# Performance work log

Hardware: AMD Instinct MI355X
Metric: run time of the kernel (lower is better)

Reference implementation:

```python
import jax, jax.numpy as jnp
import numpy as np


def setup_inputs() -> dict:
    key = jax.random.key(0)
    ks = jax.random.split(key, 8)
    B, T, D, H = 4, 4096, 1024, 64
    scale = D ** -0.5
    return {
        "x": jax.random.normal(ks[0], (B, T, D), dtype=jnp.float32),
        "mask": jax.random.randint(ks[1], (B, T), 0, 2, dtype=jnp.int32),
        "wq": jax.random.normal(ks[2], (H, D), dtype=jnp.float32) * scale,
        "bq": jax.random.normal(ks[3], (H,), dtype=jnp.float32) * 0.02,
        "wk": jax.random.normal(ks[4], (H, D), dtype=jnp.float32) * scale,
        "bk": jax.random.normal(ks[5], (H,), dtype=jnp.float32) * 0.02,
        "wv": jax.random.normal(ks[6], (H, D), dtype=jnp.float32) * scale,
        "bv": jax.random.normal(ks[7], (H,), dtype=jnp.float32) * 0.02,
    }


def reference(x, mask, wq, bq, wk, bk, wv, bv):
    # x: [B,T,D]; wq/wk/wv: [H,D] (torch Linear convention), mask: [B,T] int
    head_size = wq.shape[0]
    q = jnp.einsum("btd,hd->bth", x, wq) + bq  # [B,T,H]
    k = jnp.einsum("btd,hd->bth", x, wk) + bk
    v = jnp.einsum("btd,hd->bth", x, wv) + bv
    attn = jnp.einsum("bth,bsh->bts", q, k) * (head_size ** -0.5)  # [B,T,T]
    pad_mask = mask.astype(bool)[:, None, :]  # [B,1,T], True = keep
    attn = jnp.where(pad_mask, attn, jnp.float32(-1e9))
    attn = jax.nn.softmax(attn, axis=-1)
    # dropout is identity in eval/deterministic mode
    return jnp.einsum("bts,bsh->bth", attn, v)  # [B,T,H]
```

## Files before the change

kernel.cpp:

```cpp
#include <hip/hip_runtime.h>
#include <math.h>

#define BATCH 4
#define SEQ   4096
#define DIM   1024
#define HEAD  64
#define MROWS (BATCH*SEQ)
#define NCOL  192
#define WST   1040
#define KT    64
#define QBLK  64
#define BK2   64
#define NIT2  (DIM / BK2)

typedef __attribute__((ext_vector_type(8))) short short8;
typedef __attribute__((ext_vector_type(4))) float f32x4;

static __device__ __forceinline__ unsigned short f2b(float f) {
    union { float f; unsigned u; } v; v.f = f;
    return (unsigned short)((v.u + 0x7FFFu + ((v.u >> 16) & 1u)) >> 16);
}
static __device__ __forceinline__ unsigned cvtpk(float a, float b) {
    unsigned r;
    asm("v_cvt_pk_bf16_f32 %0, %1, %2" : "=v"(r) : "v"(a), "v"(b));
    return r;
}

#define QSC (0.125f * 1.4426950408889634f)
__global__ __launch_bounds__(256) void wconv_kernel(
    const float* __restrict__ wq, const float* __restrict__ bq,
    const float* __restrict__ wk, const float* __restrict__ bk,
    const float* __restrict__ wv, const float* __restrict__ bv,
    unsigned short* __restrict__ Wb, float* __restrict__ biasAll)
{
    int idx = blockIdx.x * 256 + threadIdx.x;
    int e   = idx * 4;
    int row = e >> 10;
    int col = e & 1023;
    const float* src = (row < 64) ? wq : (row < 128) ? wk : wv;
    float s = (row < 64) ? QSC : 1.0f;
    float4 g = *(const float4*)&src[(size_t)(row & 63) * DIM + col];
    ushort4 o;
    o.x = f2b(g.x * s); o.y = f2b(g.y * s); o.z = f2b(g.z * s); o.w = f2b(g.w * s);
    *(ushort4*)&Wb[(size_t)row * WST + col] = o;
    if (idx < 192) {
        const float* bs = (idx < 64) ? bq : (idx < 128) ? bk : bv;
        biasAll[idx] = bs[idx & 63] * ((idx < 64) ? QSC : 1.0f);
    }
}

__global__ __launch_bounds__(256, 4) void qkvmm_kernel(
    const float* __restrict__ x, const unsigned short* __restrict__ Wb,
    const float* __restrict__ biasAll,
    unsigned short* __restrict__ qout, unsigned short* __restrict__ kout,
    unsigned short* __restrict__ vtout)
{
    __shared__ unsigned short xs[32 * BK2];
    __shared__ unsigned short ws[NCOL * BK2];

    const int tid  = threadIdx.x;
    const int m0   = blockIdx.x * 32;
    const int bb   = m0 >> 12;
    const int lane = tid & 63;
    const int w    = tid >> 6;
    const int lr   = lane & 15;
    const int lg   = lane >> 4;
    const int mrow  = (w >> 1) * 16;
    const int nbase = (w & 1) * 6;

    int wrow[6], wc[6];
    #pragma unroll
    for (int j = 0; j < 6; ++j) { int L = j * 256 + tid; wrow[j] = L >> 3; wc[j] = L & 7; }
    const int xr = tid >> 2, xq = tid & 3;

    f32x4 acc[6];
    #pragma unroll
    for (int nt = 0; nt < 6; ++nt) acc[nt] = (f32x4){0.f, 0.f, 0.f, 0.f};

    float4 xg[4];
    short8 wg[6];

    auto LOADR = [&](int ko) {
        if (tid < 128) {
            const float* xp = &x[(size_t)(m0 + xr) * DIM + ko + xq * 16];
            xg[0] = *(const float4*)xp;       xg[1] = *(const float4*)(xp + 4);
            xg[2] = *(const float4*)(xp + 8); xg[3] = *(const float4*)(xp + 12);
        }
        #pragma unroll
        for (int j = 0; j < 6; ++j)
            wg[j] = *(const short8*)&Wb[(size_t)wrow[j] * WST + ko + wc[j] * 8];
    };
    auto WRITE = [&]() {
        if (tid < 128) {
            uint4 c0, c1;
            c0.x = cvtpk(xg[0].x, xg[0].y); c0.y = cvtpk(xg[0].z, xg[0].w);
            c0.z = cvtpk(xg[1].x, xg[1].y); c0.w = cvtpk(xg[1].z, xg[1].w);
            c1.x = cvtpk(xg[2].x, xg[2].y); c1.y = cvtpk(xg[2].z, xg[2].w);
            c1.z = cvtpk(xg[3].x, xg[3].y); c1.w = cvtpk(xg[3].z, xg[3].w);
            *(uint4*)&xs[xr * BK2 + (((2 * xq)     ^ (xr & 7)) * 8)] = c0;
            *(uint4*)&xs[xr * BK2 + (((2 * xq + 1) ^ (xr & 7)) * 8)] = c1;
        }
        #pragma unroll
        for (int j = 0; j < 6; ++j)
            *(short8*)&ws[wrow[j] * BK2 + ((wc[j] ^ (wrow[j] & 7)) * 8)] = wg[j];
    };

    LOADR(0);
    for (int it = 0; it < NIT2; ++it) {
        __syncthreads();
        WRITE();
        __syncthreads();
        if (it + 1 < NIT2) LOADR((it + 1) * BK2);

        __builtin_amdgcn_s_setprio(1);
        #pragma unroll
        for (int h = 0; h < 2; ++h) {
            const int arow = mrow + lr;
            short8 af = *(const short8*)&xs[arow * BK2 + (((h * 4 + lg) ^ (arow & 7)) * 8)];
            #pragma unroll
            for (int nt = 0; nt < 6; ++nt) {
                int n = (nbase + nt) * 16 + lr;
                short8 bf = *(const short8*)&ws[n * BK2 + (((h * 4 + lg) ^ (n & 7)) * 8)];
                acc[nt] = __builtin_amdgcn_mfma_f32_16x16x32_bf16(af, bf, acc[nt], 0, 0, 0);
            }
        }
        __builtin_amdgcn_s_setprio(0);
    }

    #pragma unroll
    for (int nt = 0; nt < 6; ++nt) {
        int gn = (nbase + nt) * 16 + lr;
        float bv_ = biasAll[gn];
        #pragma unroll
        for (int r = 0; r < 4; ++r) {
            int grow = m0 + mrow + lg * 4 + r;
            unsigned short val = f2b(acc[nt][r] + bv_);
            if (gn < 64)       qout[(size_t)grow * HEAD + gn] = val;
            else if (gn < 128) kout[(size_t)grow * HEAD + gn - 64] = val;
            else {
                int t = (m0 & 4095) + mrow + lg * 4 + r;
                vtout[((size_t)bb * HEAD + gn - 128) * SEQ + t] = val;
            }
        }
    }
}

__global__ __launch_bounds__(256, 4) void flashmm_kernel(
    const unsigned short* __restrict__ qb, const unsigned short* __restrict__ kb,
    const unsigned short* __restrict__ vt, const int* __restrict__ mask,
    float* __restrict__ opart, float* __restrict__ mpart, float* __restrict__ lpart,
    int nsplit)
{
    const int b  = blockIdx.y;
    const int t0 = blockIdx.x * QBLK;
    const int z  = blockIdx.z;
    const int tid  = threadIdx.x;
    const int lane = tid & 63;
    const int w    = tid >> 6;
    const int lr = lane & 15;
    const int lg = lane >> 4;
    const int span = SEQ / nsplit;
    const int s_begin = z * span, s_end = s_begin + span;

    __shared__ unsigned short ks_l[KT * HEAD];
    __shared__ unsigned short vt_l[HEAD * KT];
    __shared__ unsigned short ps_l[4][16 * KT];
    __shared__ float mkf[KT];

    const unsigned short* qrow = qb + ((size_t)(b * SEQ + t0 + w * 16 + lr)) * HEAD;
    const short8 qf0 = *(const short8*)(qrow + lg * 8);
    const short8 qf1 = *(const short8*)(qrow + 32 + lg * 8);

    f32x4 acc_o[4];
    #pragma unroll
    for (int nt = 0; nt < 4; ++nt) acc_o[nt] = (f32x4){0.f, 0.f, 0.f, 0.f};
    float m_r = -INFINITY, l_r = 0.f;

    short8 kg[2], vg[2];
    float mgf = 0.f;

    auto LOADR = [&](int st) {
        #pragma unroll
        for (int i = 0; i < 2; ++i) {
            int c   = tid + i * 256;
            int row = c >> 3;
            int h0  = (c & 7) * 8;
            kg[i] = *(const short8*)(kb + ((size_t)(b * SEQ + st + row)) * HEAD + h0);
            vg[i] = *(const short8*)(vt + ((size_t)(b * HEAD + row)) * SEQ + st + h0);
        }
        if (tid < KT) mgf = (mask[(size_t)b * SEQ + st + tid] != 0) ? 0.f : -1e9f;
    };
    auto WRITE = [&]() {
        #pragma unroll
        for (int i = 0; i < 2; ++i) {
            int c   = tid + i * 256;
            int row = c >> 3;
            int h0  = (c & 7) * 8;
            *(short8*)&ks_l[row * HEAD + (h0 ^ ((row & 7) << 3))] = kg[i];
            *(short8*)&vt_l[row * KT + (h0 ^ ((row & 7) << 3))] = vg[i];
        }
        if (tid < KT) mkf[tid] = mgf;
    };

    LOADR(s_begin);
    for (int st = s_begin; st < s_end; st += KT) {
        __syncthreads();
        WRITE();
        __syncthreads();
        if (st + KT < s_end) LOADR(st + KT);

        f32x4 sT[4];
        __builtin_amdgcn_s_setprio(1);
        #pragma unroll
        for (int ct = 0; ct < 4; ++ct) {
            int krow = ct * 16 + lr;
            short8 kf0 = *(const short8*)&ks_l[krow * HEAD + ((lg * 8) ^ ((krow & 7) << 3))];
            short8 kf1 = *(const short8*)&ks_l[krow * HEAD + ((32 + lg * 8) ^ ((krow & 7) << 3))];
            f32x4 zz = (f32x4){0.f, 0.f, 0.f, 0.f};
            zz = __builtin_amdgcn_mfma_f32_16x16x32_bf16(kf0, qf0, zz, 0, 0, 0);
            zz = __builtin_amdgcn_mfma_f32_16x16x32_bf16(kf1, qf1, zz, 0, 0, 0);
            sT[ct] = zz;
        }
        __builtin_amdgcn_s_setprio(0);

        #pragma unroll
        for (int ct = 0; ct < 4; ++ct) {
            f32x4 mb = *(const f32x4*)&mkf[ct * 16 + lg * 4];
            sT[ct][0] += mb[0]; sT[ct][1] += mb[1];
            sT[ct][2] += mb[2]; sT[ct][3] += mb[3];
        }

        float mx = sT[0][0];
        #pragma unroll
        for (int ct = 0; ct < 4; ++ct)
            #pragma unroll
            for (int r = 0; r < 4; ++r) mx = fmaxf(mx, sT[ct][r]);
        mx = fmaxf(mx, __shfl_xor(mx, 16));
        mx = fmaxf(mx, __shfl_xor(mx, 32));

        bool defer = __all(mx <= m_r + 8.f);
        float base = defer ? m_r : fmaxf(m_r, mx);

        float rs = 0.f;
        #pragma unroll
        for (int ct = 0; ct < 4; ++ct)
            #pragma unroll
            for (int r = 0; r < 4; ++r) {
                float p = __builtin_amdgcn_exp2f(sT[ct][r] - base);
                sT[ct][r] = p;
                rs += p;
            }
        rs += __shfl_xor(rs, 16);
        rs += __shfl_xor(rs, 32);

        if (defer) {
            l_r += rs;
        } else {
            float sf = __builtin_amdgcn_exp2f(m_r - base);
            l_r = l_r * sf + rs;
            m_r = base;
            #pragma unroll
            for (int r = 0; r < 4; ++r) {
                float sfr = __shfl(sf, lg * 4 + r);
                #pragma unroll
                for (int nt = 0; nt < 4; ++nt) acc_o[nt][r] *= sfr;
            }
        }

        #pragma unroll
        for (int ct = 0; ct < 4; ++ct) {
            uint2 pk;
            pk.x = cvtpk(sT[ct][0], sT[ct][1]);
            pk.y = cvtpk(sT[ct][2], sT[ct][3]);
            *(uint2*)&ps_l[w][lr * KT + ((ct * 16 + lg * 4) ^ ((lr & 7) << 3))] = pk;
        }

        __builtin_amdgcn_s_setprio(1);
        #pragma unroll
        for (int kk = 0; kk < 2; ++kk) {
            int s0 = kk * 32 + lg * 8;
            short8 pf = *(const short8*)&ps_l[w][lr * KT + (s0 ^ ((lr & 7) << 3))];
            #pragma unroll
            for (int nt = 0; nt < 4; ++nt) {
                int hrow = nt * 16 + lr;
                short8 vf = *(const short8*)&vt_l[hrow * KT + (s0 ^ ((hrow & 7) << 3))];
                acc_o[nt] = __builtin_amdgcn_mfma_f32_16x16x32_bf16(pf, vf, acc_o[nt], 0, 0, 0);
            }
        }
        __builtin_amdgcn_s_setprio(0);
    }

    const size_t rbase = (size_t)z * MROWS + (size_t)b * SEQ + t0 + w * 16;
    const size_t obase = rbase * HEAD;
    #pragma unroll
    for (int nt = 0; nt < 4; ++nt)
        #pragma unroll
        for (int r = 0; r < 4; ++r) {
            int R = lg * 4 + r;
            opart[obase + (size_t)R * HEAD + nt * 16 + lr] = acc_o[nt][r];
        }
    if (lg == 0) {
        mpart[rbase + lr] = m_r;
        lpart[rbase + lr] = l_r;
    }
}

__global__ __launch_bounds__(256) void combine_kernel(
    const float* __restrict__ op, const float* __restrict__ mp,
    const float* __restrict__ lp, float* __restrict__ out, int nsplit)
{
    int idx = blockIdx.x * 256 + threadIdx.x;
    int row = idx >> 4;
    int h4  = (idx & 15) * 4;
    float mstar = -INFINITY;
    for (int s = 0; s < nsplit; ++s)
        mstar = fmaxf(mstar, mp[(size_t)s * MROWS + row]);
    float L = 0.f;
    float ax = 0.f, ay = 0.f, az = 0.f, aw = 0.f;
    for (int s = 0; s < nsplit; ++s) {
        float wgt = __builtin_amdgcn_exp2f(mp[(size_t)s * MROWS + row] - mstar);
        L += lp[(size_t)s * MROWS + row] * wgt;
        float4 o = *(const float4*)&op[((size_t)s * MROWS + row) * HEAD + h4];
        ax += o.x * wgt; ay += o.y * wgt; az += o.z * wgt; aw += o.w * wgt;
    }
    float r = 1.f / L;
    float4 res; res.x = ax * r; res.y = ay * r; res.z = az * r; res.w = aw * r;
    *(float4*)&out[(size_t)row * HEAD + h4] = res;
}

extern "C" void kernel_launch(void* const* d_in, const int* in_sizes, int n_in,
                              void* d_out, int out_size, void* d_ws, size_t ws_size,
                              hipStream_t stream) {
    const float* x    = (const float*)d_in[0];
    const int*   mask = (const int*)d_in[1];
    const float* wq   = (const float*)d_in[2];
    const float* bq   = (const float*)d_in[3];
    const float* wk   = (const float*)d_in[4];
    const float* bk   = (const float*)d_in[5];
    const float* wv   = (const float*)d_in[6];
    const float* bv   = (const float*)d_in[7];
    float* out = (float*)d_out;
    (void)in_sizes; (void)n_in; (void)out_size;

    const size_t NB = (size_t)MROWS * HEAD;
    unsigned short* qw  = (unsigned short*)d_ws;
    unsigned short* kw  = qw + NB;
    unsigned short* vtw = kw + NB;
    unsigned short* Wb  = vtw + NB;
    float* biasAll = (float*)(Wb + (size_t)NCOL * WST);
    float* mpart   = biasAll + 192;

    const size_t base = 3 * NB * 2 + (size_t)NCOL * WST * 2 + 192 * 4;
    const size_t per  = (size_t)MROWS * 8 + NB * 4;
    int KS = 1;
    if      (ws_size >= base + 4 * per) KS = 4;
    else if (ws_size >= base + 2 * per) KS = 2;

    float* lpart = mpart + (size_t)KS * MROWS;
    float* opart = lpart + (size_t)KS * MROWS;

    wconv_kernel<<<dim3(192), 256, 0, stream>>>(wq, bq, wk, bk, wv, bv, Wb, biasAll);
    qkvmm_kernel<<<dim3(MROWS / 32), 256, 0, stream>>>(x, Wb, biasAll, qw, kw, vtw);
    flashmm_kernel<<<dim3(SEQ / QBLK, BATCH, KS), 256, 0, stream>>>(qw, kw, vtw, mask,
                                                                    opart, mpart, lpart, KS);
    combine_kernel<<<dim3(MROWS * 16 / 256), 256, 0, stream>>>(opart, mpart, lpart, out, KS);
}
```

Baseline: 74.44 us.

## Give each flash-attention wave two 16-row query tiles with 128-thread blocks

The attention kernel drops to 2 waves per block, and each wave now handles 32 query rows as two 16-row sub-tiles. Every K and V fragment read from shared memory feeds two MFMAs, which halves LDS reads per MFMA and raises MFMA density per wave. The cost is more registers per thread (double accumulators, scores and Q fragments), a lower occupancy hint, and fewer threads to share the global tile loads.

```diff
diff --git a/kernel.cpp b/kernel.cpp
--- a/kernel.cpp
+++ b/kernel.cpp
@@ -145,7 +145,7 @@
     }
 }
 
-__global__ __launch_bounds__(256, 4) void flashmm_kernel(
+__global__ __launch_bounds__(128, 3) void flashmm_kernel(
     const unsigned short* __restrict__ qb, const unsigned short* __restrict__ kb,
     const unsigned short* __restrict__ vt, const int* __restrict__ mask,
     float* __restrict__ opart, float* __restrict__ mpart, float* __restrict__ lpart,
@@ -164,25 +164,33 @@
 
     __shared__ unsigned short ks_l[KT * HEAD];
     __shared__ unsigned short vt_l[HEAD * KT];
-    __shared__ unsigned short ps_l[4][16 * KT];
+    __shared__ unsigned short ps_l[2][2][16 * KT];
     __shared__ float mkf[KT];
 
-    const unsigned short* qrow = qb + ((size_t)(b * SEQ + t0 + w * 16 + lr)) * HEAD;
-    const short8 qf0 = *(const short8*)(qrow + lg * 8);
-    const short8 qf1 = *(const short8*)(qrow + 32 + lg * 8);
-
-    f32x4 acc_o[4];
-    #pragma unroll
-    for (int nt = 0; nt < 4; ++nt) acc_o[nt] = (f32x4){0.f, 0.f, 0.f, 0.f};
-    float m_r = -INFINITY, l_r = 0.f;
-
-    short8 kg[2], vg[2];
+    short8 qf[2][2];
+    #pragma unroll
+    for (int u = 0; u < 2; ++u) {
+        const unsigned short* qrow =
+            qb + ((size_t)(b * SEQ + t0 + w * 32 + u * 16 + lr)) * HEAD;
+        qf[u][0] = *(const short8*)(qrow + lg * 8);
+        qf[u][1] = *(const short8*)(qrow + 32 + lg * 8);
+    }
+
+    f32x4 acc_o[2][4];
+    #pragma unroll
+    for (int u = 0; u < 2; ++u)
+        #pragma unroll
+        for (int nt = 0; nt < 4; ++nt) acc_o[u][nt] = (f32x4){0.f, 0.f, 0.f, 0.f};
+    float m_r[2] = {-INFINITY, -INFINITY};
+    float l_r[2] = {0.f, 0.f};
+
+    short8 kg[4], vg[4];
     float mgf = 0.f;
 
     auto LOADR = [&](int st) {
         #pragma unroll
-        for (int i = 0; i < 2; ++i) {
-            int c   = tid + i * 256;
+        for (int i = 0; i < 4; ++i) {
+            int c   = tid + i * 128;
             int row = c >> 3;
             int h0  = (c & 7) * 8;
             kg[i] = *(const short8*)(kb + ((size_t)(b * SEQ + st + row)) * HEAD + h0);
@@ -192,8 +200,8 @@
     };
     auto WRITE = [&]() {
         #pragma unroll
-        for (int i = 0; i < 2; ++i) {
-            int c   = tid + i * 256;
+        for (int i = 0; i < 4; ++i) {
+            int c   = tid + i * 128;
             int row = c >> 3;
             int h0  = (c & 7) * 8;
             *(short8*)&ks_l[row * HEAD + (h0 ^ ((row & 7) << 3))] = kg[i];
@@ -209,99 +217,113 @@
         __syncthreads();
         if (st + KT < s_end) LOADR(st + KT);
 
-        f32x4 sT[4];
+        f32x4 sT[2][4];
         __builtin_amdgcn_s_setprio(1);
         #pragma unroll
         for (int ct = 0; ct < 4; ++ct) {
             int krow = ct * 16 + lr;
             short8 kf0 = *(const short8*)&ks_l[krow * HEAD + ((lg * 8) ^ ((krow & 7) << 3))];
             short8 kf1 = *(const short8*)&ks_l[krow * HEAD + ((32 + lg * 8) ^ ((krow & 7) << 3))];
-            f32x4 zz = (f32x4){0.f, 0.f, 0.f, 0.f};
-            zz = __builtin_amdgcn_mfma_f32_16x16x32_bf16(kf0, qf0, zz, 0, 0, 0);
-            zz = __builtin_amdgcn_mfma_f32_16x16x32_bf16(kf1, qf1, zz, 0, 0, 0);
-            sT[ct] = zz;
+            #pragma unroll
+            for (int u = 0; u < 2; ++u) {
+                f32x4 zz = (f32x4){0.f, 0.f, 0.f, 0.f};
+                zz = __builtin_amdgcn_mfma_f32_16x16x32_bf16(kf0, qf[u][0], zz, 0, 0, 0);
+                zz = __builtin_amdgcn_mfma_f32_16x16x32_bf16(kf1, qf[u][1], zz, 0, 0, 0);
+                sT[u][ct] = zz;
+            }
         }
         __builtin_amdgcn_s_setprio(0);
 
         #pragma unroll
         for (int ct = 0; ct < 4; ++ct) {
             f32x4 mb = *(const f32x4*)&mkf[ct * 16 + lg * 4];
-            sT[ct][0] += mb[0]; sT[ct][1] += mb[1];
-            sT[ct][2] += mb[2]; sT[ct][3] += mb[3];
-        }
-
-        float mx = sT[0][0];
-        #pragma unroll
-        for (int ct = 0; ct < 4; ++ct)
-            #pragma unroll
-            for (int r = 0; r < 4; ++r) mx = fmaxf(mx, sT[ct][r]);
-        mx = fmaxf(mx, __shfl_xor(mx, 16));
-        mx = fmaxf(mx, __shfl_xor(mx, 32));
-
-        bool defer = __all(mx <= m_r + 8.f);
-        float base = defer ? m_r : fmaxf(m_r, mx);
-
-        float rs = 0.f;
-        #pragma unroll
-        for (int ct = 0; ct < 4; ++ct)
-            #pragma unroll
-            for (int r = 0; r < 4; ++r) {
-                float p = __builtin_amdgcn_exp2f(sT[ct][r] - base);
-                sT[ct][r] = p;
-                rs += p;
-            }
-        rs += __shfl_xor(rs, 16);
-        rs += __shfl_xor(rs, 32);
-
-        if (defer) {
-            l_r += rs;
-        } else {
-            float sf = __builtin_amdgcn_exp2f(m_r - base);
-            l_r = l_r * sf + rs;
-            m_r = base;
-            #pragma unroll
-            for (int r = 0; r < 4; ++r) {
-                float sfr = __shfl(sf, lg * 4 + r);
+            #pragma unroll
+            for (int u = 0; u < 2; ++u) {
+                sT[u][ct][0] += mb[0]; sT[u][ct][1] += mb[1];
+                sT[u][ct][2] += mb[2]; sT[u][ct][3] += mb[3];
+            }
+        }
+
+        #pragma unroll
+        for (int u = 0; u < 2; ++u) {
+            float mx = sT[u][0][0];
+            #pragma unroll
+            for (int ct = 0; ct < 4; ++ct)
                 #pragma unroll
-                for (int nt = 0; nt < 4; ++nt) acc_o[nt][r] *= sfr;
-            }
-        }
-
-        #pragma unroll
-        for (int ct = 0; ct < 4; ++ct) {
-            uint2 pk;
-            pk.x = cvtpk(sT[ct][0], sT[ct][1]);
-            pk.y = cvtpk(sT[ct][2], sT[ct][3]);
-            *(uint2*)&ps_l[w][lr * KT + ((ct * 16 + lg * 4) ^ ((lr & 7) << 3))] = pk;
+                for (int r = 0; r < 4; ++r) mx = fmaxf(mx, sT[u][ct][r]);
+            mx = fmaxf(mx, __shfl_xor(mx, 16));
+            mx = fmaxf(mx, __shfl_xor(mx, 32));
+
+            bool defer = __all(mx <= m_r[u] + 8.f);
+            float base = defer ? m_r[u] : fmaxf(m_r[u], mx);
+
+            float rs = 0.f;
+            #pragma unroll
+            for (int ct = 0; ct < 4; ++ct)
+                #pragma unroll
+                for (int r = 0; r < 4; ++r) {
+                    float p = __builtin_amdgcn_exp2f(sT[u][ct][r] - base);
+                    sT[u][ct][r] = p;
+                    rs += p;
+                }
+            rs += __shfl_xor(rs, 16);
+            rs += __shfl_xor(rs, 32);
+
+            if (defer) {
+                l_r[u] += rs;
+            } else {
+                float sf = __builtin_amdgcn_exp2f(m_r[u] - base);
+                l_r[u] = l_r[u] * sf + rs;
+                m_r[u] = base;
+                #pragma unroll
+                for (int r = 0; r < 4; ++r) {
+                    float sfr = __shfl(sf, lg * 4 + r);
+                    #pragma unroll
+                    for (int nt = 0; nt < 4; ++nt) acc_o[u][nt][r] *= sfr;
+                }
+            }
+
+            #pragma unroll
+            for (int ct = 0; ct < 4; ++ct) {
+                uint2 pk;
+                pk.x = cvtpk(sT[u][ct][0], sT[u][ct][1]);
+                pk.y = cvtpk(sT[u][ct][2], sT[u][ct][3]);
+                *(uint2*)&ps_l[w][u][lr * KT + ((ct * 16 + lg * 4) ^ ((lr & 7) << 3))] = pk;
+            }
         }
 
         __builtin_amdgcn_s_setprio(1);
         #pragma unroll
         for (int kk = 0; kk < 2; ++kk) {
             int s0 = kk * 32 + lg * 8;
-            short8 pf = *(const short8*)&ps_l[w][lr * KT + (s0 ^ ((lr & 7) << 3))];
+            short8 pf0 = *(const short8*)&ps_l[w][0][lr * KT + (s0 ^ ((lr & 7) << 3))];
+            short8 pf1 = *(const short8*)&ps_l[w][1][lr * KT + (s0 ^ ((lr & 7) << 3))];
             #pragma unroll
             for (int nt = 0; nt < 4; ++nt) {
                 int hrow = nt * 16 + lr;
                 short8 vf = *(const short8*)&vt_l[hrow * KT + (s0 ^ ((hrow & 7) << 3))];
-                acc_o[nt] = __builtin_amdgcn_mfma_f32_16x16x32_bf16(pf, vf, acc_o[nt], 0, 0, 0);
+                acc_o[0][nt] = __builtin_amdgcn_mfma_f32_16x16x32_bf16(pf0, vf, acc_o[0][nt], 0, 0, 0);
+                acc_o[1][nt] = __builtin_amdgcn_mfma_f32_16x16x32_bf16(pf1, vf, acc_o[1][nt], 0, 0, 0);
             }
         }
         __builtin_amdgcn_s_setprio(0);
     }
 
-    const size_t rbase = (size_t)z * MROWS + (size_t)b * SEQ + t0 + w * 16;
-    const size_t obase = rbase * HEAD;
-    #pragma unroll
-    for (int nt = 0; nt < 4; ++nt)
-        #pragma unroll
-        for (int r = 0; r < 4; ++r) {
-            int R = lg * 4 + r;
-            opart[obase + (size_t)R * HEAD + nt * 16 + lr] = acc_o[nt][r];
-        }
-    if (lg == 0) {
-        mpart[rbase + lr] = m_r;
-        lpart[rbase + lr] = l_r;
+    #pragma unroll
+    for (int u = 0; u < 2; ++u) {
+        const size_t rbase = (size_t)z * MROWS + (size_t)b * SEQ + t0 + w * 32 + u * 16;
+        const size_t obase = rbase * HEAD;
+        #pragma unroll
+        for (int nt = 0; nt < 4; ++nt)
+            #pragma unroll
+            for (int r = 0; r < 4; ++r) {
+                int R = lg * 4 + r;
+                opart[obase + (size_t)R * HEAD + nt * 16 + lr] = acc_o[u][nt][r];
+            }
+        if (lg == 0) {
+            mpart[rbase + lr] = m_r[u];
+            lpart[rbase + lr] = l_r[u];
+        }
     }
 }
 
@@ -361,7 +383,7 @@
 
     wconv_kernel<<<dim3(192), 256, 0, stream>>>(wq, bq, wk, bk, wv, bv, Wb, biasAll);
     qkvmm_kernel<<<dim3(MROWS / 32), 256, 0, stream>>>(x, Wb, biasAll, qw, kw, vtw);
-    flashmm_kernel<<<dim3(SEQ / QBLK, BATCH, KS), 256, 0, stream>>>(qw, kw, vtw, mask,
+    flashmm_kernel<<<dim3(SEQ / QBLK, BATCH, KS), 128, 0, stream>>>(qw, kw, vtw, mask,
                                                                     opart, mpart, lpart, KS);
     combine_kernel<<<dim3(MROWS * 16 / 256), 256, 0, stream>>>(opart, mpart, lpart, out, KS);
 }
```

Result: slower. 122.8 us (+65.0%).
